# Kernel tuning notes

Hardware: AMD Instinct MI355X
Metric: run time of the kernel (lower is better)

Reference implementation:

```python
import jax, jax.numpy as jnp
import numpy as np

B, S, D, H, W = 2, 2048, 1024, 16, 128
HD = D // H
EPS = 1e-5
NEG = -1e9


def setup_inputs() -> dict:
    key = jax.random.key(0)
    ks = jax.random.split(key, 6)
    sd = 1.0 / np.sqrt(D)
    return {
        "x": jax.random.normal(ks[0], (B, S, D), jnp.float32),
        "Wq": jax.random.normal(ks[1], (D, D), jnp.float32) * sd,
        "bq": jnp.zeros((D,), jnp.float32),
        "Wk": jax.random.normal(ks[2], (D, D), jnp.float32) * sd,
        "bk": jnp.zeros((D,), jnp.float32),
        "Wv": jax.random.normal(ks[3], (D, D), jnp.float32) * sd,
        "bv": jnp.zeros((D,), jnp.float32),
        "Wo": jax.random.normal(ks[4], (D, D), jnp.float32) * sd,
        "bo": jnp.zeros((D,), jnp.float32),
        "gamma": jnp.ones((D,), jnp.float32),
        "beta": jnp.zeros((D,), jnp.float32),
    }


def _local_causal_mask(seq_len, window):
    pos = jnp.arange(seq_len)
    qp = pos[:, None]
    kp = pos[None, :]
    return (jnp.abs(qp - kp) < window) & (qp >= kp)  # [S, S] bool


def reference(x, Wq, bq, Wk, bk, Wv, bv, Wo, bo, gamma, beta):
    scale = 1.0 / np.sqrt(HD)
    # projections -> [B, H, S, HD]
    def split_heads(t):
        return t.reshape(B, S, H, HD).transpose(0, 2, 1, 3)

    q = split_heads(x @ Wq + bq)
    k = split_heads(x @ Wk + bk)
    v = split_heads(x @ Wv + bv)

    scores = jnp.einsum("bhqd,bhkd->bhqk", q, k) * scale  # [B,H,S,S]
    mask = _local_causal_mask(S, W)
    scores = jnp.where(mask[None, None, :, :], scores, NEG)
    attn = jax.nn.softmax(scores, axis=-1)
    out = jnp.einsum("bhqk,bhkd->bhqd", attn, v)  # [B,H,S,HD]
    out = out.transpose(0, 2, 1, 3).reshape(B, S, D)
    out = out @ Wo + bo

    # residual + LayerNorm(eps=1e-5)
    y = x + out
    mu = jnp.mean(y, axis=-1, keepdims=True)
    var = jnp.mean(jnp.square(y - mu), axis=-1, keepdims=True)
    y = (y - mu) * jax.lax.rsqrt(var + EPS) * gamma + beta
    return y
```

## Files before the change

### kernel.cpp

```cpp
#include <hip/hip_runtime.h>
#include <hip/hip_bf16.h>

typedef __hip_bfloat16 bf16;
typedef float f32x4 __attribute__((ext_vector_type(4)));
typedef short bf16x8 __attribute__((ext_vector_type(8)));
typedef int   int4v  __attribute__((ext_vector_type(4)));

constexpr int Bb = 2, Ss = 2048, Dd = 1024, Hh = 16, Ww = 128, HDd = 64;
constexpr int Mrows = Bb * Ss;
constexpr int NTk = Dd / 64;

__device__ __forceinline__ void gload16(const void* g, void* l) {
  __builtin_amdgcn_global_load_lds(
      (const __attribute__((address_space(1))) void*)g,
      (__attribute__((address_space(3))) void*)l, 16, 0, 0);
}

__device__ __forceinline__ f32x4 mfma16(bf16x8 a, bf16x8 b, f32x4 c) {
  return __builtin_amdgcn_mfma_f32_16x16x32_bf16(a, b, c, 0, 0, 0);
}

__global__ __launch_bounds__(256) void convert_bf16_k(const float* __restrict__ in,
                                                      bf16* __restrict__ out) {
  size_t i = (size_t)blockIdx.x * 256 + threadIdx.x;
  float4 v = reinterpret_cast<const float4*>(in)[i];
  union { bf16 b[4]; ushort4 u; } cv;
  cv.b[0] = __float2bfloat16(v.x);
  cv.b[1] = __float2bfloat16(v.y);
  cv.b[2] = __float2bfloat16(v.z);
  cv.b[3] = __float2bfloat16(v.w);
  reinterpret_cast<ushort4*>(out)[i] = cv.u;
}

__global__ __launch_bounds__(256) void transpose_w4_k(const float* __restrict__ W0,
                                                      const float* __restrict__ W1,
                                                      const float* __restrict__ W2,
                                                      const float* __restrict__ W3,
                                                      bf16* __restrict__ out) {
  const float* Win = (blockIdx.z == 0) ? W0 : (blockIdx.z == 1) ? W1
                     : (blockIdx.z == 2) ? W2 : W3;
  bf16* o = out + (size_t)blockIdx.z * Dd * Dd;
  __shared__ float tile[32][33];
  int bx = blockIdx.x, by = blockIdx.y;
  int tx = threadIdx.x & 31, ty = threadIdx.x >> 5;
#pragma unroll
  for (int i = 0; i < 4; ++i)
    tile[ty + i * 8][tx] = Win[(size_t)(by * 32 + ty + i * 8) * Dd + bx * 32 + tx];
  __syncthreads();
#pragma unroll
  for (int i = 0; i < 4; ++i)
    o[(size_t)(bx * 32 + ty + i * 8) * Dd + by * 32 + tx] =
        __float2bfloat16(tile[tx][ty + i * 8]);
}

__device__ __forceinline__ void gemm_core8(const bf16* __restrict__ A,
                                           const bf16* __restrict__ Bt,
                                           int bm, int bn,
                                           bf16* lds, f32x4 acc[2][4]) {
  const int t = threadIdx.x;
  const int lane = t & 63, w = t >> 6;
  const int wr = w >> 1, wc = w & 1;
  const int l15 = lane & 15, l16 = lane >> 4;
  const bf16* Arow0 = A + (size_t)bm * 128 * Dd;
  const bf16* Brow0 = Bt + (size_t)bn * 128 * Dd;

  auto stage = [&](int buf, int kt) {
#pragma unroll
    for (int i = 0; i < 2; ++i) {
      int ci = i * 512 + t;
      int row = ci >> 3, pc = ci & 7;
      int sc = pc ^ (row & 7);
      gload16(Arow0 + (size_t)row * Dd + kt * 64 + sc * 8, lds + buf * 16384 + ci * 8);
      gload16(Brow0 + (size_t)row * Dd + kt * 64 + sc * 8, lds + buf * 16384 + 8192 + ci * 8);
    }
  };

  stage(0, 0);
  __syncthreads();
  int buf = 0;
  for (int kt = 0; kt < NTk; ++kt) {
    if (kt + 1 < NTk) stage(buf ^ 1, kt + 1);
    bf16x8 af[2][2], bfr[4][2];
    const bf16* Ab = lds + buf * 16384;
    const bf16* Bb = Ab + 8192;
#pragma unroll
    for (int m = 0; m < 2; ++m) {
      int row = wr * 32 + m * 16 + l15;
#pragma unroll
      for (int kk = 0; kk < 2; ++kk)
        af[m][kk] = *reinterpret_cast<const bf16x8*>(
            Ab + row * 64 + (((kk * 4 + l16) ^ (row & 7)) * 8));
    }
#pragma unroll
    for (int n = 0; n < 4; ++n) {
      int row = wc * 64 + n * 16 + l15;
#pragma unroll
      for (int kk = 0; kk < 2; ++kk)
        bfr[n][kk] = *reinterpret_cast<const bf16x8*>(
            Bb + row * 64 + (((kk * 4 + l16) ^ (row & 7)) * 8));
    }
    __builtin_amdgcn_s_setprio(1);
#pragma unroll
    for (int m = 0; m < 2; ++m)
#pragma unroll
      for (int n = 0; n < 4; ++n) {
        acc[m][n] = mfma16(af[m][0], bfr[n][0], acc[m][n]);
        acc[m][n] = mfma16(af[m][1], bfr[n][1], acc[m][n]);
      }
    __builtin_amdgcn_s_setprio(0);
    __syncthreads();
    buf ^= 1;
  }
}

__global__ __launch_bounds__(512) void gemm_qkv8w(const bf16* __restrict__ A,
                                                  const bf16* __restrict__ Wt3,
                                                  const float* __restrict__ bq,
                                                  const float* __restrict__ bk,
                                                  const float* __restrict__ bv,
                                                  bf16* __restrict__ Qh,
                                                  bf16* __restrict__ Kh,
                                                  bf16* __restrict__ Vt) {
  __shared__ __align__(16) bf16 lds[32768];
  f32x4 acc[2][4] = {};
  int id = blockIdx.x;
  int wg = (id & 7) * 96 + (id >> 3);
  int bm = wg / 24, bn = wg % 24;
  gemm_core8(A, Wt3, bm, bn, lds, acc);

  const int lane = threadIdx.x & 63, w = threadIdx.x >> 6;
  const int wr = w >> 1, wc = w & 1, l15 = lane & 15, l16 = lane >> 4;
  const int p = bn >> 3;
  const int c0w = (bn & 7) * 128 + wc * 64;
  const int h = c0w >> 6;

  if (p < 2) {
    bf16 (*rep)[72] = reinterpret_cast<bf16(*)[72]>(lds + w * (16 * 72));
    bf16* dst = p ? Kh : Qh;
    const float* bp = p ? bk : bq;
    float bi[4];
#pragma unroll
    for (int n = 0; n < 4; ++n) bi[n] = bp[c0w + n * 16 + l15];
#pragma unroll
    for (int m = 0; m < 2; ++m) {
#pragma unroll
      for (int n = 0; n < 4; ++n)
#pragma unroll
        for (int r = 0; r < 4; ++r)
          rep[l16 * 4 + r][n * 16 + l15] = __float2bfloat16(acc[m][n][r] + bi[n]);
      int rrow = lane >> 2, rch = lane & 3;
      int sg = bm * 128 + wr * 32 + m * 16 + rrow;
      int b = sg >> 11, sl = sg & (Ss - 1);
      bf16* base = dst + (((size_t)(b * Hh + h)) * Ss + sl) * HDd;
      bf16x8 v0 = *reinterpret_cast<const bf16x8*>(&rep[rrow][rch * 8]);
      bf16x8 v1 = *reinterpret_cast<const bf16x8*>(&rep[rrow][(rch + 4) * 8]);
      *reinterpret_cast<bf16x8*>(base + rch * 8) = v0;
      *reinterpret_cast<bf16x8*>(base + (rch + 4) * 8) = v1;
    }
  } else {
#pragma unroll
    for (int n = 0; n < 4; ++n) {
      int col = c0w + n * 16 + l15;
      int hh = col >> 6, hd = col & (HDd - 1);
      float bi = bv[col];
#pragma unroll
      for (int m = 0; m < 2; ++m) {
        int s0 = bm * 128 + wr * 32 + m * 16 + l16 * 4;
        int b = s0 >> 11, sl = s0 & (Ss - 1);
        union { ushort4 u; ushort e[4]; } pk;
#pragma unroll
        for (int r = 0; r < 4; ++r) {
          bf16 tb = __float2bfloat16(acc[m][n][r] + bi);
          pk.e[r] = *reinterpret_cast<ushort*>(&tb);
        }
        *reinterpret_cast<ushort4*>(&Vt[(((size_t)(b * Hh + hh)) * HDd + hd) * Ss + sl]) = pk.u;
      }
    }
  }
}

__global__ __launch_bounds__(512) void gemm_o8w(const bf16* __restrict__ AO,
                                                const bf16* __restrict__ WtO,
                                                const float* __restrict__ bo,
                                                const float* __restrict__ resid,
                                                float* __restrict__ out) {
  __shared__ __align__(16) bf16 lds[32768];
  f32x4 acc[2][4] = {};
  int id = blockIdx.x;
  int wg = (id & 7) * 32 + (id >> 3);
  int bm = wg >> 3, bn = wg & 7;
  gemm_core8(AO, WtO, bm, bn, lds, acc);

  const int lane = threadIdx.x & 63, w = threadIdx.x >> 6;
  const int wr = w >> 1, wc = w & 1, l15 = lane & 15, l16 = lane >> 4;
#pragma unroll
  for (int m = 0; m < 2; ++m)
#pragma unroll
    for (int n = 0; n < 4; ++n) {
      int col = bn * 128 + wc * 64 + n * 16 + l15;
      float bi = bo[col];
#pragma unroll
      for (int r = 0; r < 4; ++r) {
        int row = bm * 128 + wr * 32 + m * 16 + l16 * 4 + r;
        size_t idx = (size_t)row * Dd + col;
        out[idx] = acc[m][n][r] + bi + resid[idx];
      }
    }
}

__global__ __launch_bounds__(512) void attn_local2(const bf16* __restrict__ Q,
                                                   const bf16* __restrict__ K,
                                                   const bf16* __restrict__ Vt,
                                                   bf16* __restrict__ AO) {
  __shared__ __align__(16) bf16 Kl[256 * 64];
  __shared__ bf16 Ps[8][16][168];
  const int t = threadIdx.x, lane = t & 63, w = t >> 6;
  const int l15 = lane & 15, l16 = lane >> 4;
  const int qb = blockIdx.x, h = blockIdx.y, b = blockIdx.z;
  const int q0 = qb * 128, kstart = q0 - 128;
  const bf16* Qp = Q + ((size_t)(b * Hh + h)) * Ss * HDd;
  const bf16* Kp = K + ((size_t)(b * Hh + h)) * Ss * HDd;
  const bf16* Vp = Vt + ((size_t)(b * Hh + h)) * HDd * Ss;

#pragma unroll
  for (int i = 0; i < 4; ++i) {
    int ci = i * 512 + t;
    int row = ci >> 3, pc = ci & 7;
    int sc = pc ^ (row & 7);
    int key = kstart + row;
    if (key < 0) key = 0;
    gload16(Kp + (size_t)key * HDd + sc * 8, (bf16*)Kl + ci * 8);
  }

  const int qrow = q0 + w * 16 + l15;
  bf16x8 aq0 = *reinterpret_cast<const bf16x8*>(Qp + (size_t)qrow * HDd + l16 * 8);
  bf16x8 aq1 = *reinterpret_cast<const bf16x8*>(Qp + (size_t)qrow * HDd + 32 + l16 * 8);

  __syncthreads();

  f32x4 sc9[9];
  __builtin_amdgcn_s_setprio(1);
#pragma unroll
  for (int j = 0; j < 9; ++j) {
    int krow = (w + j) * 16 + l15;
    bf16x8 bk0 = *reinterpret_cast<const bf16x8*>(
        Kl + krow * 64 + (((0 + l16) ^ (krow & 7)) * 8));
    bf16x8 bk1 = *reinterpret_cast<const bf16x8*>(
        Kl + krow * 64 + (((4 + l16) ^ (krow & 7)) * 8));
    f32x4 s = {};
    s = mfma16(aq0, bk0, s);
    s = mfma16(aq1, bk1, s);
    sc9[j] = s;
  }
  __builtin_amdgcn_s_setprio(0);

  const float scale = 0.125f;
  float mrow[4], ssum[4], inv[4];
  int qg[4];
#pragma unroll
  for (int r = 0; r < 4; ++r) { mrow[r] = -1e30f; qg[r] = q0 + w * 16 + l16 * 4 + r; }
#pragma unroll
  for (int j = 0; j < 9; ++j) {
    int kg = kstart + (w + j) * 16 + l15;
#pragma unroll
    for (int r = 0; r < 4; ++r) {
      bool valid = (kg >= 0) && (kg <= qg[r]) && (qg[r] - kg < Ww);
      float v = valid ? sc9[j][r] * scale : -1e9f;
      sc9[j][r] = v;
      mrow[r] = fmaxf(mrow[r], v);
    }
  }
#pragma unroll
  for (int r = 0; r < 4; ++r)
#pragma unroll
    for (int off = 1; off < 16; off <<= 1)
      mrow[r] = fmaxf(mrow[r], __shfl_xor(mrow[r], off));
#pragma unroll
  for (int r = 0; r < 4; ++r) ssum[r] = 0.f;
#pragma unroll
  for (int j = 0; j < 9; ++j)
#pragma unroll
    for (int r = 0; r < 4; ++r) {
      float p = __expf(sc9[j][r] - mrow[r]);
      sc9[j][r] = p;
      ssum[r] += p;
    }
#pragma unroll
  for (int r = 0; r < 4; ++r)
#pragma unroll
    for (int off = 1; off < 16; off <<= 1)
      ssum[r] += __shfl_xor(ssum[r], off);
#pragma unroll
  for (int r = 0; r < 4; ++r) inv[r] = 1.f / ssum[r];

#pragma unroll
  for (int j = 0; j < 9; ++j) {
    int lt = j + (w & 1);
#pragma unroll
    for (int r = 0; r < 4; ++r)
      Ps[w][l16 * 4 + r][lt * 16 + l15] = __float2bfloat16(sc9[j][r]);
  }
  {
    int ltz = (w & 1) ? 0 : 9;
    bf16 z16 = __float2bfloat16(0.f);
#pragma unroll
    for (int r = 0; r < 4; ++r)
      Ps[w][l16 * 4 + r][ltz * 16 + l15] = z16;
  }

  f32x4 o[4] = {};
  __builtin_amdgcn_s_setprio(1);
#pragma unroll
  for (int cc = 0; cc < 5; ++cc) {
    bf16x8 pf = *reinterpret_cast<const bf16x8*>(&Ps[w][l15][cc * 32 + l16 * 8]);
    int kk = kstart + ((w >> 1) + cc) * 32 + l16 * 8;
    int kc = kk < 0 ? 0 : kk;
#pragma unroll
    for (int ht = 0; ht < 4; ++ht) {
      bf16x8 vf = *reinterpret_cast<const bf16x8*>(Vp + (size_t)(ht * 16 + l15) * Ss + kc);
      o[ht] = mfma16(pf, vf, o[ht]);
    }
  }
  __builtin_amdgcn_s_setprio(0);

#pragma unroll
  for (int ht = 0; ht < 4; ++ht)
#pragma unroll
    for (int r = 0; r < 4; ++r) {
      int qw = q0 + w * 16 + l16 * 4 + r;
      int col = h * HDd + ht * 16 + l15;
      AO[(size_t)(b * Ss + qw) * Dd + col] = __float2bfloat16(o[ht][r] * inv[r]);
    }
}

__global__ __launch_bounds__(256) void ln_inplace(float* __restrict__ y,
                                                  const float* __restrict__ gamma,
                                                  const float* __restrict__ beta) {
  int row = blockIdx.x;
  float* yr = y + (size_t)row * Dd;
  float4 v = reinterpret_cast<const float4*>(yr)[threadIdx.x];
  float s = v.x + v.y + v.z + v.w;
  float s2 = v.x * v.x + v.y * v.y + v.z * v.z + v.w * v.w;
#pragma unroll
  for (int off = 1; off < 64; off <<= 1) {
    s += __shfl_xor(s, off);
    s2 += __shfl_xor(s2, off);
  }
  __shared__ float r1[4], r2[4];
  int w = threadIdx.x >> 6;
  if ((threadIdx.x & 63) == 0) { r1[w] = s; r2[w] = s2; }
  __syncthreads();
  s = r1[0] + r1[1] + r1[2] + r1[3];
  s2 = r2[0] + r2[1] + r2[2] + r2[3];
  float mu = s * (1.f / Dd);
  float var = s2 * (1.f / Dd) - mu * mu;
  float rs = rsqrtf(var + 1e-5f);
  float4 g = reinterpret_cast<const float4*>(gamma)[threadIdx.x];
  float4 be = reinterpret_cast<const float4*>(beta)[threadIdx.x];
  float4 o;
  o.x = (v.x - mu) * rs * g.x + be.x;
  o.y = (v.y - mu) * rs * g.y + be.y;
  o.z = (v.z - mu) * rs * g.z + be.z;
  o.w = (v.w - mu) * rs * g.w + be.w;
  reinterpret_cast<float4*>(yr)[threadIdx.x] = o;
}

extern "C" void kernel_launch(void* const* d_in, const int* in_sizes, int n_in,
                              void* d_out, int out_size, void* d_ws, size_t ws_size,
                              hipStream_t stream) {
  const float* x     = (const float*)d_in[0];
  const float* Wq    = (const float*)d_in[1];
  const float* bq    = (const float*)d_in[2];
  const float* Wk    = (const float*)d_in[3];
  const float* bk    = (const float*)d_in[4];
  const float* Wv    = (const float*)d_in[5];
  const float* bv    = (const float*)d_in[6];
  const float* Wo    = (const float*)d_in[7];
  const float* bo    = (const float*)d_in[8];
  const float* gamma = (const float*)d_in[9];
  const float* beta  = (const float*)d_in[10];
  float* out = (float*)d_out;

  char* ws = (char*)d_ws;
  bf16* xb  = (bf16*)(ws + (size_t)0);
  bf16* Wt3 = (bf16*)(ws + ((size_t)8  << 20));
  bf16* WtO = (bf16*)(ws + ((size_t)14 << 20));
  bf16* Qh  = (bf16*)(ws + ((size_t)16 << 20));
  bf16* Kh  = (bf16*)(ws + ((size_t)24 << 20));
  bf16* Vt  = (bf16*)(ws + ((size_t)32 << 20));
  bf16* AO  = (bf16*)(ws + ((size_t)40 << 20));

  convert_bf16_k<<<Mrows * Dd / (256 * 4), 256, 0, stream>>>(x, xb);
  transpose_w4_k<<<dim3(32, 32, 4), 256, 0, stream>>>(Wq, Wk, Wv, Wo, Wt3);

  gemm_qkv8w<<<768, 512, 0, stream>>>(xb, Wt3, bq, bk, bv, Qh, Kh, Vt);

  attn_local2<<<dim3(Ss / 128, Hh, Bb), 512, 0, stream>>>(Qh, Kh, Vt, AO);

  gemm_o8w<<<256, 512, 0, stream>>>(AO, WtO, bo, x, out);
  ln_inplace<<<Mrows, 256, 0, stream>>>(out, gamma, beta);
}
```

Measured before the change: 90.54 us.

## Split GEMM K-tile across wave halves with LDS partial-sum reduction

```diff
diff --git a/kernel.cpp b/kernel.cpp
--- a/kernel.cpp
+++ b/kernel.cpp
@@ -53,13 +53,13 @@
         __float2bfloat16(tile[tx][ty + i * 8]);
 }
 
-__device__ __forceinline__ void gemm_core8(const bf16* __restrict__ A,
-                                           const bf16* __restrict__ Bt,
-                                           int bm, int bn,
-                                           bf16* lds, f32x4 acc[2][4]) {
+__device__ __forceinline__ void gemm_core8p(const bf16* __restrict__ A,
+                                            const bf16* __restrict__ Bt,
+                                            int bm, int bn,
+                                            bf16* lds, f32x4 acc[4][4]) {
   const int t = threadIdx.x;
   const int lane = t & 63, w = t >> 6;
-  const int wr = w >> 1, wc = w & 1;
+  const int q = w & 3, qr = q >> 1, qc = q & 1, kh = w >> 2;
   const int l15 = lane & 15, l16 = lane >> 4;
   const bf16* Arow0 = A + (size_t)bm * 128 * Dd;
   const bf16* Brow0 = Bt + (size_t)bn * 128 * Dd;
@@ -80,36 +80,51 @@
   int buf = 0;
   for (int kt = 0; kt < NTk; ++kt) {
     if (kt + 1 < NTk) stage(buf ^ 1, kt + 1);
-    bf16x8 af[2][2], bfr[4][2];
     const bf16* Ab = lds + buf * 16384;
     const bf16* Bb = Ab + 8192;
-#pragma unroll
-    for (int m = 0; m < 2; ++m) {
-      int row = wr * 32 + m * 16 + l15;
-#pragma unroll
-      for (int kk = 0; kk < 2; ++kk)
-        af[m][kk] = *reinterpret_cast<const bf16x8*>(
-            Ab + row * 64 + (((kk * 4 + l16) ^ (row & 7)) * 8));
+    bf16x8 af[4], bfr[4];
+#pragma unroll
+    for (int m = 0; m < 4; ++m) {
+      int row = qr * 64 + m * 16 + l15;
+      af[m] = *reinterpret_cast<const bf16x8*>(
+          Ab + row * 64 + (((kh * 4 + l16) ^ (row & 7)) * 8));
     }
 #pragma unroll
     for (int n = 0; n < 4; ++n) {
-      int row = wc * 64 + n * 16 + l15;
-#pragma unroll
-      for (int kk = 0; kk < 2; ++kk)
-        bfr[n][kk] = *reinterpret_cast<const bf16x8*>(
-            Bb + row * 64 + (((kk * 4 + l16) ^ (row & 7)) * 8));
+      int row = qc * 64 + n * 16 + l15;
+      bfr[n] = *reinterpret_cast<const bf16x8*>(
+          Bb + row * 64 + (((kh * 4 + l16) ^ (row & 7)) * 8));
     }
     __builtin_amdgcn_s_setprio(1);
 #pragma unroll
-    for (int m = 0; m < 2; ++m)
-#pragma unroll
-      for (int n = 0; n < 4; ++n) {
-        acc[m][n] = mfma16(af[m][0], bfr[n][0], acc[m][n]);
-        acc[m][n] = mfma16(af[m][1], bfr[n][1], acc[m][n]);
-      }
+    for (int m = 0; m < 4; ++m)
+#pragma unroll
+      for (int n = 0; n < 4; ++n)
+        acc[m][n] = mfma16(af[m], bfr[n], acc[m][n]);
     __builtin_amdgcn_s_setprio(0);
     __syncthreads();
     buf ^= 1;
+  }
+
+  float* part = reinterpret_cast<float*>(lds);
+  if (kh == 1) {
+    float* base = part + q * 4096;
+#pragma unroll
+    for (int m = 0; m < 4; ++m)
+#pragma unroll
+      for (int n = 0; n < 4; ++n)
+        *reinterpret_cast<f32x4*>(base + (m * 4 + n) * 256 + lane * 4) = acc[m][n];
+  }
+  __syncthreads();
+  if (kh == 0) {
+    float* base = part + q * 4096;
+#pragma unroll
+    for (int m = 0; m < 4; ++m)
+#pragma unroll
+      for (int n = 0; n < 4; ++n) {
+        f32x4 p = *reinterpret_cast<const f32x4*>(base + (m * 4 + n) * 256 + lane * 4);
+        acc[m][n] += p;
+      }
   }
 }
 
@@ -122,34 +137,35 @@
                                                   bf16* __restrict__ Kh,
                                                   bf16* __restrict__ Vt) {
   __shared__ __align__(16) bf16 lds[32768];
-  f32x4 acc[2][4] = {};
+  f32x4 acc[4][4] = {};
   int id = blockIdx.x;
   int wg = (id & 7) * 96 + (id >> 3);
   int bm = wg / 24, bn = wg % 24;
-  gemm_core8(A, Wt3, bm, bn, lds, acc);
+  gemm_core8p(A, Wt3, bm, bn, lds, acc);
 
   const int lane = threadIdx.x & 63, w = threadIdx.x >> 6;
-  const int wr = w >> 1, wc = w & 1, l15 = lane & 15, l16 = lane >> 4;
+  if (w >= 4) return;
+  const int qr = (w >> 1) & 1, qc = w & 1, l15 = lane & 15, l16 = lane >> 4;
   const int p = bn >> 3;
-  const int c0w = (bn & 7) * 128 + wc * 64;
+  const int c0w = (bn & 7) * 128 + qc * 64;
   const int h = c0w >> 6;
 
   if (p < 2) {
-    bf16 (*rep)[72] = reinterpret_cast<bf16(*)[72]>(lds + w * (16 * 72));
+    bf16 (*rep)[72] = reinterpret_cast<bf16(*)[72]>(lds + w * 8192);
     bf16* dst = p ? Kh : Qh;
     const float* bp = p ? bk : bq;
     float bi[4];
 #pragma unroll
     for (int n = 0; n < 4; ++n) bi[n] = bp[c0w + n * 16 + l15];
 #pragma unroll
-    for (int m = 0; m < 2; ++m) {
+    for (int m = 0; m < 4; ++m) {
 #pragma unroll
       for (int n = 0; n < 4; ++n)
 #pragma unroll
         for (int r = 0; r < 4; ++r)
           rep[l16 * 4 + r][n * 16 + l15] = __float2bfloat16(acc[m][n][r] + bi[n]);
       int rrow = lane >> 2, rch = lane & 3;
-      int sg = bm * 128 + wr * 32 + m * 16 + rrow;
+      int sg = bm * 128 + qr * 64 + m * 16 + rrow;
       int b = sg >> 11, sl = sg & (Ss - 1);
       bf16* base = dst + (((size_t)(b * Hh + h)) * Ss + sl) * HDd;
       bf16x8 v0 = *reinterpret_cast<const bf16x8*>(&rep[rrow][rch * 8]);
@@ -164,8 +180,8 @@
       int hh = col >> 6, hd = col & (HDd - 1);
       float bi = bv[col];
 #pragma unroll
-      for (int m = 0; m < 2; ++m) {
-        int s0 = bm * 128 + wr * 32 + m * 16 + l16 * 4;
+      for (int m = 0; m < 4; ++m) {
+        int s0 = bm * 128 + qr * 64 + m * 16 + l16 * 4;
         int b = s0 >> 11, sl = s0 & (Ss - 1);
         union { ushort4 u; ushort e[4]; } pk;
 #pragma unroll
@@ -185,23 +201,24 @@
                                                 const float* __restrict__ resid,
                                                 float* __restrict__ out) {
   __shared__ __align__(16) bf16 lds[32768];
-  f32x4 acc[2][4] = {};
+  f32x4 acc[4][4] = {};
   int id = blockIdx.x;
   int wg = (id & 7) * 32 + (id >> 3);
   int bm = wg >> 3, bn = wg & 7;
-  gemm_core8(AO, WtO, bm, bn, lds, acc);
+  gemm_core8p(AO, WtO, bm, bn, lds, acc);
 
   const int lane = threadIdx.x & 63, w = threadIdx.x >> 6;
-  const int wr = w >> 1, wc = w & 1, l15 = lane & 15, l16 = lane >> 4;
-#pragma unroll
-  for (int m = 0; m < 2; ++m)
+  if (w >= 4) return;
+  const int qr = (w >> 1) & 1, qc = w & 1, l15 = lane & 15, l16 = lane >> 4;
+#pragma unroll
+  for (int m = 0; m < 4; ++m)
 #pragma unroll
     for (int n = 0; n < 4; ++n) {
-      int col = bn * 128 + wc * 64 + n * 16 + l15;
+      int col = bn * 128 + qc * 64 + n * 16 + l15;
       float bi = bo[col];
 #pragma unroll
       for (int r = 0; r < 4; ++r) {
-        int row = bm * 128 + wr * 32 + m * 16 + l16 * 4 + r;
+        int row = bm * 128 + qr * 64 + m * 16 + l16 * 4 + r;
         size_t idx = (size_t)row * Dd + col;
         out[idx] = acc[m][n][r] + bi + resid[idx];
       }
```

Result: slower. 94.48 us (+4.3%).
